# Performance work log

Hardware: AMD Instinct MI355X
Metric: run time of the kernel (lower is better)

## Reference

```python
import jax, jax.numpy as jnp
import numpy as np

GAMMA = 1.0
BIG = 1e30  # finite stand-in for +inf to keep gradients NaN-free


def pairwise_sqdist(x, y):
    # x: [B, C, N], y: [B, C, M] -> [B, N, M] squared euclidean distances
    xx = jnp.sum(x * x, axis=1)                      # [B, N]
    yy = jnp.sum(y * y, axis=1)                      # [B, M]
    xy = jnp.einsum('bcn,bcm->bnm', x, y)            # [B, N, M]
    return xx[:, :, None] + yy[:, None, :] - 2.0 * xy


def soft_dtw(D, gamma):
    # Anti-diagonal wavefront soft-DTW DP.
    # R[i, j] = D[i-1, j-1] + softmin(R[i-1,j-1], R[i-1,j], R[i,j-1])
    # Diagonal d = i + j; store diag as [B, N+1] arrays indexed by i.
    B, N, M = D.shape
    i_idx = jnp.arange(N + 1)
    # d = 0 diagonal: R[0,0] = 0, everything else +inf
    diag0 = jnp.full((B, N + 1), BIG, D.dtype).at[:, 0].set(0.0)
    # d = 1 diagonal: R[1,0] and R[0,1] are +inf
    diag1 = jnp.full((B, N + 1), BIG, D.dtype)

    def step(carry, d):
        prev2, prev1 = carry                      # diagonals d-2, d-1
        j = d - i_idx                             # 1-based column index
        valid = (i_idx >= 1) & (i_idx <= N) & (j >= 1) & (j <= M)
        di = jnp.clip(i_idx - 1, 0, N - 1)
        dj = jnp.clip(j - 1, 0, M - 1)
        dvals = D[:, di, dj]                      # [B, N+1]
        r0 = jnp.roll(prev2, 1, axis=1)           # R[i-1, j-1]
        r1 = jnp.roll(prev1, 1, axis=1)           # R[i-1, j]
        r2 = prev1                                # R[i, j-1]
        stacked = jnp.stack([r0, r1, r2], axis=0)  # [3, B, N+1]
        softmin = -gamma * jax.nn.logsumexp(-stacked / gamma, axis=0)
        cur = jnp.where(valid[None, :], dvals + softmin, BIG)
        return (prev1, cur), None

    ds = jnp.arange(2, N + M + 1)
    (_, last), _ = jax.lax.scan(step, (diag0, diag1), ds)
    return last[:, N]                             # R[N, M] per batch


def setup_inputs() -> dict:
    key = jax.random.key(0)
    kx, ky = jax.random.split(key)
    B, C, N = 32, 80, 512
    x = jax.random.normal(kx, (B, C, N), dtype=jnp.float32)
    y = jax.random.normal(ky, (B, C, N), dtype=jnp.float32)
    return {"x": x, "y": y}


def reference(x, y):
    D = pairwise_sqdist(x, y)     # save_memory=True path
    return soft_dtw(D, GAMMA)     # [B], normalize=False; squeeze(0) is a no-op
```

## Files before the change

kernel.cpp:

```cpp
#include <hip/hip_runtime.h>
#include <hip/hip_bf16.h>

#define BIGF 1e30f
#define TC 80
#define TN 512
#define L2E 1.4426950408889634f
#define LN2 0.6931471805599453f

typedef float f32x2 __attribute__((ext_vector_type(2)));
typedef float f32x4 __attribute__((ext_vector_type(4)));
typedef __attribute__((address_space(1))) const unsigned int gu32;
typedef __attribute__((address_space(3))) unsigned int lu32;

__global__ __launch_bounds__(256) void pairdist_kernel(
    const float* __restrict__ x, const float* __restrict__ y,
    float* __restrict__ F) {
  const int b  = blockIdx.z;
  const int n0 = blockIdx.x * 128;
  const int m0 = blockIdx.y * 128;

  __shared__ float xs[40][128];
  __shared__ float ys[40][128];
  __shared__ float xxs[128];
  __shared__ float yys[128];

  const float* xb = x + (size_t)b * TC * TN;
  const float* yb = y + (size_t)b * TC * TN;
  const int tid = threadIdx.x;
  const int tm = tid & 15, tn = tid >> 4;
  const int nc = tid & 127;
  const bool isX = tid < 128;

  float acc[8][8] = {};
  float nrm = 0.f;

  for (int half = 0; half < 2; ++half) {
    const int c0 = half * 40;
    for (int idx = tid; idx < 1280; idx += 256) {
      int c = idx >> 5, q = idx & 31;
      *(float4*)&xs[c][q * 4] =
          *(const float4*)&xb[(size_t)(c0 + c) * TN + n0 + q * 4];
      *(float4*)&ys[c][q * 4] =
          *(const float4*)&yb[(size_t)(c0 + c) * TN + m0 + q * 4];
    }
    __syncthreads();

    if (isX) {
      for (int c = 0; c < 40; ++c) { float v = xs[c][nc]; nrm += v * v; }
    } else {
      for (int c = 0; c < 40; ++c) { float v = ys[c][nc]; nrm += v * v; }
    }

    for (int c = 0; c < 40; ++c) {
      float4 xa0 = *(const float4*)&xs[c][tn * 8];
      float4 xa1 = *(const float4*)&xs[c][tn * 8 + 4];
      float4 ya0 = *(const float4*)&ys[c][tm * 8];
      float4 ya1 = *(const float4*)&ys[c][tm * 8 + 4];
      float xv[8] = {xa0.x, xa0.y, xa0.z, xa0.w, xa1.x, xa1.y, xa1.z, xa1.w};
      float yv[8] = {ya0.x, ya0.y, ya0.z, ya0.w, ya1.x, ya1.y, ya1.z, ya1.w};
#pragma unroll
      for (int a2 = 0; a2 < 8; ++a2)
#pragma unroll
        for (int q2 = 0; q2 < 8; ++q2) acc[a2][q2] += xv[a2] * yv[q2];
    }
    __syncthreads();
  }

  if (isX) xxs[nc] = nrm; else yys[nc] = nrm;
  __syncthreads();

  float* Fb = F + (size_t)b * TN * TN;
  const int i0 = m0 + tm * 8;
  const int v0 = i0 >> 1;
#pragma unroll
  for (int a = 0; a < 8; ++a) {
    int jj = n0 + tn * 8 + a;
    float xxv = xxs[tn * 8 + a];
#pragma unroll
    for (int k = 0; k < 4; ++k) {
      float2 o;
      o.x = (xxv + yys[tm * 8 + 2 * k]     - 2.f * acc[a][2 * k])     * L2E;
      o.y = (xxv + yys[tm * 8 + 2 * k + 1] - 2.f * acc[a][2 * k + 1]) * L2E;
      int p = (jj + v0 + k) & (TN - 1);
      *(float2*)&Fb[(size_t)p * TN + i0 + 2 * k] = o;
    }
  }
}

__global__ __launch_bounds__(256) __attribute__((amdgpu_waves_per_eu(1)))
void sdtw_kernel(const float* __restrict__ Ft, float* __restrict__ out) {
  const int b   = blockIdx.x;
  const int tid = threadIdx.x;
  const int g   = tid & 63;
  const int w   = tid >> 6;
  const float* Fb = Ft + (size_t)b * TN * TN;

  __shared__ float ring[4][8][128];
  __shared__ f32x4 hand[3][2][2];

  if (tid < 12) {
    f32x4 iv; iv[0] = BIGF; iv[1] = BIGF; iv[2] = BIGF; iv[3] = BIGF;
    ((f32x4*)hand)[tid] = iv;
  }
  __syncthreads();

  float p0 = BIGF, p1 = BIGF;
  float up_p = (tid == 0) ? 0.f : BIGF;

  auto stage = [&](int slot, int u) {
    const float* gp =
        Fb + (size_t)((u - 7 * w) & (TN - 1)) * TN + w * 128 + g;
    __builtin_amdgcn_global_load_lds((gu32*)gp,        (lu32*)&ring[w][slot][0],  4, 0, 0);
    __builtin_amdgcn_global_load_lds((gu32*)(gp + 64), (lu32*)&ring[w][slot][64], 4, 0, 0);
  };

  const unsigned rbase =
      (unsigned)(size_t)(__attribute__((address_space(3))) float*)&ring[w][0][0];
  const unsigned hbase =
      (unsigned)(size_t)(__attribute__((address_space(3))) f32x4*)&hand[0][0];

  auto cell = [&](float d, float r0, float r1, float r2) -> float {
    float mn, md, mx;
    asm("v_min3_f32 %0, %3, %4, %5\n\t"
        "v_med3_f32 %1, %3, %4, %5\n\t"
        "v_max3_f32 %2, %3, %4, %5"
        : "=&v"(mn), "=&v"(md), "=&v"(mx)
        : "v"(r0), "v"(r1), "v"(r2));
    float e1 = __builtin_amdgcn_exp2f(mn - md);
    float e2 = __builtin_amdgcn_exp2f(mn - mx);
    float dm = d + mn;
    float ss = (1.0f + e1) + e2;
    return dm - __builtin_amdgcn_logf(ss);
  };

  auto body = [&](f32x2 d, float pubk) -> float {
    float upc = __int_as_float(__builtin_amdgcn_update_dpp(
        __float_as_int(pubk), __float_as_int(p1), 0x138, 0xf, 0xf, false));
    float c0 = cell(d[0], up_p, upc, p0);
    float c1 = cell(d[1], p0, c0, p1);
    p0 = c0; p1 = c1; up_p = upc;
    return c1;
  };

  stage(0, 0); stage(1, 1); stage(2, 2); stage(3, 3);
  stage(4, 4); stage(5, 5); stage(6, 6); stage(7, 7);

  f32x2 d0, d1, d2, d3, d4, d5, d6, d7;

  int s = 0;
  for (int B = 0; B < 98; ++B, s += 8) {
    __builtin_amdgcn_s_barrier();
    asm volatile("s_waitcnt vmcnt(0)" ::: "memory");

    unsigned ad = rbase + (unsigned)(g * 8);
    asm volatile(
        "ds_read_b64 %0, %8\n\t"
        "ds_read_b64 %1, %8 offset:512\n\t"
        "ds_read_b64 %2, %8 offset:1024\n\t"
        "ds_read_b64 %3, %8 offset:1536\n\t"
        "ds_read_b64 %4, %8 offset:2048\n\t"
        "ds_read_b64 %5, %8 offset:2560\n\t"
        "ds_read_b64 %6, %8 offset:3072\n\t"
        "ds_read_b64 %7, %8 offset:3584\n\t"
        "s_waitcnt lgkmcnt(0)"
        : "=&v"(d0), "=&v"(d1), "=&v"(d2), "=&v"(d3),
          "=&v"(d4), "=&v"(d5), "=&v"(d6), "=&v"(d7)
        : "v"(ad)
        : "memory");

    f32x4 pA, pB;
    if (w > 0) {
      unsigned ha = hbase + (unsigned)(((w - 1) * 2 + ((B + 1) & 1)) * 32);
      asm volatile("ds_read_b128 %0, %2\n\t"
                   "ds_read_b128 %1, %2 offset:16\n\t"
                   "s_waitcnt lgkmcnt(0)"
                   : "=&v"(pA), "=&v"(pB) : "v"(ha) : "memory");
    } else {
      pA[0] = pA[1] = pA[2] = pA[3] = BIGF;
      pB[0] = pB[1] = pB[2] = pB[3] = BIGF;
    }

    stage(0, s + 8);  stage(1, s + 9);
    stage(2, s + 10); stage(3, s + 11);
    stage(4, s + 12); stage(5, s + 13);
    stage(6, s + 14); stage(7, s + 15);

    f32x4 k0, k1;
    k0[0] = body(d0, pA[0]); k0[1] = body(d1, pA[1]);
    k0[2] = body(d2, pA[2]); k0[3] = body(d3, pA[3]);
    k1[0] = body(d4, pB[0]); k1[1] = body(d5, pB[1]);
    k1[2] = body(d6, pB[2]); k1[3] = body(d7, pB[3]);

    if (w < 3 && g == 63) {
      unsigned wa = hbase + (unsigned)((w * 2 + (B & 1)) * 32);
      asm volatile("ds_write_b128 %0, %1\n\t"
                   "ds_write_b128 %0, %2 offset:16\n\t"
                   "s_waitcnt lgkmcnt(0)"
                   :: "v"(wa), "v"(k0), "v"(k1) : "memory");
    }
  }

  __builtin_amdgcn_s_barrier();
  asm volatile("s_waitcnt vmcnt(0)" ::: "memory");
  {
    unsigned ad = rbase + (unsigned)(g * 8);
    asm volatile(
        "ds_read_b64 %0, %4\n\t"
        "ds_read_b64 %1, %4 offset:512\n\t"
        "ds_read_b64 %2, %4 offset:1024\n\t"
        "ds_read_b64 %3, %4 offset:1536\n\t"
        "s_waitcnt lgkmcnt(0)"
        : "=&v"(d0), "=&v"(d1), "=&v"(d2), "=&v"(d3)
        : "v"(ad)
        : "memory");
  }
  f32x4 pA;
  if (w > 0) {
    unsigned ha = hbase + (unsigned)(((w - 1) * 2 + 1) * 32);
    asm volatile("ds_read_b128 %0, %1\n\ts_waitcnt lgkmcnt(0)"
                 : "=&v"(pA) : "v"(ha) : "memory");
  } else {
    pA[0] = pA[1] = pA[2] = pA[3] = BIGF;
  }
  body(d0, pA[0]); body(d1, pA[1]); body(d2, pA[2]); body(d3, pA[3]);

  if (tid == 255) out[b] = p1 * LN2;
}

extern "C" void kernel_launch(void* const* d_in, const int* in_sizes, int n_in,
                              void* d_out, int out_size, void* d_ws, size_t ws_size,
                              hipStream_t stream) {
  const float* x = (const float*)d_in[0];
  const float* y = (const float*)d_in[1];
  float* out = (float*)d_out;
  float* F = (float*)d_ws;

  dim3 g1(TN / 128, TN / 128, 32);
  pairdist_kernel<<<g1, 256, 0, stream>>>(y, x, F);
  sdtw_kernel<<<32, 256, 0, stream>>>(F, out);
}
```

Measured before the change: 188.9 us.

## Compute pairwise dot products with bf16 MFMA instead of fp32 FMA tiles

Rewrites the pairwise-distance kernel to convert x/y to bf16, store them in swizzled LDS tiles, and use mfma_f32_16x16x32_bf16 for the cross term, padding C from 80 to 96. Norms are still computed in fp32 straight from global memory. The aim is to cut the fp32 FMA cost of the distance GEMM. The price is bf16 rounding of the dot product, which may shift the soft-DTW output, and per-element scalar stores in place of float2 stores. The sdtw kernel, which probably dominates the runtime, is unchanged.

```diff
diff --git a/kernel.cpp b/kernel.cpp
--- a/kernel.cpp
+++ b/kernel.cpp
@@ -9,6 +9,7 @@
 
 typedef float f32x2 __attribute__((ext_vector_type(2)));
 typedef float f32x4 __attribute__((ext_vector_type(4)));
+typedef short s16x8 __attribute__((ext_vector_type(8)));
 typedef __attribute__((address_space(1))) const unsigned int gu32;
 typedef __attribute__((address_space(3))) unsigned int lu32;
 
@@ -19,70 +20,97 @@
   const int n0 = blockIdx.x * 128;
   const int m0 = blockIdx.y * 128;
 
-  __shared__ float xs[40][128];
-  __shared__ float ys[40][128];
-  __shared__ float xxs[128];
-  __shared__ float yys[128];
+  __shared__ __align__(16) short Ab[128 * 128];
+  __shared__ __align__(16) short Bb[128 * 128];
+  __shared__ float xxs[128], yys[128];
 
   const float* xb = x + (size_t)b * TC * TN;
   const float* yb = y + (size_t)b * TC * TN;
   const int tid = threadIdx.x;
-  const int tm = tid & 15, tn = tid >> 4;
-  const int nc = tid & 127;
-  const bool isX = tid < 128;
-
-  float acc[8][8] = {};
-  float nrm = 0.f;
-
-  for (int half = 0; half < 2; ++half) {
-    const int c0 = half * 40;
-    for (int idx = tid; idx < 1280; idx += 256) {
-      int c = idx >> 5, q = idx & 31;
-      *(float4*)&xs[c][q * 4] =
-          *(const float4*)&xb[(size_t)(c0 + c) * TN + n0 + q * 4];
-      *(float4*)&ys[c][q * 4] =
-          *(const float4*)&yb[(size_t)(c0 + c) * TN + m0 + q * 4];
-    }
-    __syncthreads();
-
-    if (isX) {
-      for (int c = 0; c < 40; ++c) { float v = xs[c][nc]; nrm += v * v; }
-    } else {
-      for (int c = 0; c < 40; ++c) { float v = ys[c][nc]; nrm += v * v; }
-    }
-
-    for (int c = 0; c < 40; ++c) {
-      float4 xa0 = *(const float4*)&xs[c][tn * 8];
-      float4 xa1 = *(const float4*)&xs[c][tn * 8 + 4];
-      float4 ya0 = *(const float4*)&ys[c][tm * 8];
-      float4 ya1 = *(const float4*)&ys[c][tm * 8 + 4];
-      float xv[8] = {xa0.x, xa0.y, xa0.z, xa0.w, xa1.x, xa1.y, xa1.z, xa1.w};
-      float yv[8] = {ya0.x, ya0.y, ya0.z, ya0.w, ya1.x, ya1.y, ya1.z, ya1.w};
-#pragma unroll
-      for (int a2 = 0; a2 < 8; ++a2)
-#pragma unroll
-        for (int q2 = 0; q2 < 8; ++q2) acc[a2][q2] += xv[a2] * yv[q2];
-    }
-    __syncthreads();
-  }
-
-  if (isX) xxs[nc] = nrm; else yys[nc] = nrm;
+
+  auto sw = [](int row, int k) -> int {
+    return (row * 256 + k * 2) ^ ((row & 7) << 4);
+  };
+  auto cvt = [](float f) -> unsigned short {
+    unsigned u = __float_as_uint(f);
+    return (unsigned short)((u + 0x7FFFu + ((u >> 16) & 1u)) >> 16);
+  };
+
+  for (int item = tid; item < 12 * 128 * 2; item += 256) {
+    int arr = (item >= 12 * 128) ? 1 : 0;
+    int it  = item - arr * 12 * 128;
+    int oct = it >> 7, n = it & 127;
+    const float* src = arr ? (yb + m0 + n) : (xb + n0 + n);
+    s16x8 pk;
+#pragma unroll
+    for (int j = 0; j < 8; ++j) {
+      int c = oct * 8 + j;
+      float v = (c < TC) ? src[(size_t)c * TN] : 0.f;
+      pk[j] = (short)cvt(v);
+    }
+    short* dst = arr ? Bb : Ab;
+    *(s16x8*)((char*)dst + sw(n, oct * 8)) = pk;
+  }
+
+  if (tid < 128) {
+    float s = 0.f;
+    for (int c = 0; c < TC; ++c) {
+      float v = xb[(size_t)c * TN + n0 + tid];
+      s += v * v;
+    }
+    xxs[tid] = s;
+  } else {
+    int n = tid - 128;
+    float s = 0.f;
+    for (int c = 0; c < TC; ++c) {
+      float v = yb[(size_t)c * TN + m0 + n];
+      s += v * v;
+    }
+    yys[n] = s;
+  }
   __syncthreads();
 
+  const int l  = tid & 63;
+  const int w  = tid >> 6;
+  const int wm = (w >> 1) * 64, wn = (w & 1) * 64;
+  const int fr = l & 15;
+  const int fk = (l >> 4) * 8;
+
+  f32x4 acc[4][4] = {};
+#pragma unroll
+  for (int ks = 0; ks < 3; ++ks) {
+    const int k0 = ks * 32 + fk;
+    s16x8 af[4], bfr[4];
+#pragma unroll
+    for (int ta = 0; ta < 4; ++ta)
+      af[ta] = *(const s16x8*)((const char*)Ab + sw(wm + ta * 16 + fr, k0));
+#pragma unroll
+    for (int tq = 0; tq < 4; ++tq)
+      bfr[tq] = *(const s16x8*)((const char*)Bb + sw(wn + tq * 16 + fr, k0));
+#pragma unroll
+    for (int ta = 0; ta < 4; ++ta)
+#pragma unroll
+      for (int tq = 0; tq < 4; ++tq)
+        acc[ta][tq] = __builtin_amdgcn_mfma_f32_16x16x32_bf16(
+            af[ta], bfr[tq], acc[ta][tq], 0, 0, 0);
+  }
+
   float* Fb = F + (size_t)b * TN * TN;
-  const int i0 = m0 + tm * 8;
-  const int v0 = i0 >> 1;
-#pragma unroll
-  for (int a = 0; a < 8; ++a) {
-    int jj = n0 + tn * 8 + a;
-    float xxv = xxs[tn * 8 + a];
-#pragma unroll
-    for (int k = 0; k < 4; ++k) {
-      float2 o;
-      o.x = (xxv + yys[tm * 8 + 2 * k]     - 2.f * acc[a][2 * k])     * L2E;
-      o.y = (xxv + yys[tm * 8 + 2 * k + 1] - 2.f * acc[a][2 * k + 1]) * L2E;
-      int p = (jj + v0 + k) & (TN - 1);
-      *(float2*)&Fb[(size_t)p * TN + i0 + 2 * k] = o;
+#pragma unroll
+  for (int ta = 0; ta < 4; ++ta) {
+    const int mb = wm + ta * 16 + (l >> 4) * 4;
+#pragma unroll
+    for (int r = 0; r < 4; ++r) {
+      const int jj = n0 + mb + r;
+      const float xxv = xxs[mb + r];
+#pragma unroll
+      for (int tq = 0; tq < 4; ++tq) {
+        const int nn = wn + tq * 16 + fr;
+        const int i  = m0 + nn;
+        float val = (xxv + yys[nn] - 2.f * acc[ta][tq][r]) * L2E;
+        int p = (jj + (i >> 1)) & (TN - 1);
+        Fb[(size_t)p * TN + i] = val;
+      }
     }
   }
 }
```

New measurement: 177.2 us. -6.2%, faster.
